# Performance work log

Hardware: AMD Instinct MI355X
Metric: run time of the kernel (lower is better)

The kernel has to match this reference:

```python
import jax, jax.numpy as jnp
import numpy as np

N = 100000
MUL_IN0, MUL_IN1 = 256, 128      # in_irreps: 256x0e + 128x1o  (dim 640)
MUL_S, MUL_G = 512, 256          # hidden: 512x0e scalars, 256x1o gated (+256x0e gates)
MUL_H0 = MUL_S + MUL_G           # 768 l=0 channels produced by lin1/lin2
MUL_OUT0, MUL_OUT1 = 256, 128    # out_irreps: 256x0e + 128x1o (dim 640)
EPS = 1e-5


def _p(key, shape):
    return jax.random.normal(key, shape, dtype=jnp.float32)


def setup_inputs() -> dict:
    key = jax.random.key(0)
    ks = jax.random.split(key, 11)
    return {
        "features": _p(ks[0], (N, MUL_IN0 + 3 * MUL_IN1)),
        "lin1_W0": _p(ks[1], (MUL_IN0, MUL_H0)),
        "lin1_W1": _p(ks[2], (MUL_IN1, MUL_G)),
        "lin2_W0": _p(ks[3], (MUL_S, MUL_H0)),
        "lin2_W1": _p(ks[4], (MUL_G, MUL_G)),
        "lin3_W0": _p(ks[5], (MUL_S, MUL_OUT0)),
        "lin3_W1": _p(ks[6], (MUL_G, MUL_OUT1)),
        "byp_W0": _p(ks[7], (MUL_IN0, MUL_OUT0)),
        "byp_W1": _p(ks[8], (MUL_IN1, MUL_OUT1)),
        "bn_weight": jnp.ones((MUL_OUT0 + MUL_OUT1,), jnp.float32),
        "bn_bias": jnp.zeros((MUL_OUT0,), jnp.float32),
    }


def _irlin(x, mul0_in, mul1_in, W0, W1):
    # e3nn o3.Linear on simplified irreps: independent (block-diagonal) matmul
    # per angular momentum l, with 1/sqrt(fan_in) path normalization.
    n = x.shape[0]
    x0 = x[:, :mul0_in]                              # [n, mul0_in]      l=0
    x1 = x[:, mul0_in:].reshape(n, mul1_in, 3)       # [n, mul1_in, 3]   l=1
    y0 = (x0 @ W0) * np.float32(1.0 / np.sqrt(mul0_in))
    y1 = jnp.einsum('nid,io->nod', x1, W1) * np.float32(1.0 / np.sqrt(mul1_in))
    return jnp.concatenate([y0, y1.reshape(n, -1)], axis=-1)


def _gate(h):
    # e3nn Gate: SiLU on scalars, sigmoid(gates) multiplies each gated l=1 irrep
    n = h.shape[0]
    s = jax.nn.silu(h[:, :MUL_S])
    g = jax.nn.sigmoid(h[:, MUL_S:MUL_S + MUL_G])
    v = h[:, MUL_S + MUL_G:].reshape(n, MUL_G, 3)
    return jnp.concatenate([s, (v * g[:, :, None]).reshape(n, -1)], axis=-1)


def _batchnorm(x, w, b):
    # e3nn BatchNorm (training mode, normalization='component', reduce='mean'):
    # scalars get mean-subtraction + bias; l>0 only per-mul norm scaling.
    n = x.shape[0]
    s = x[:, :MUL_OUT0]
    v = x[:, MUL_OUT0:].reshape(n, MUL_OUT1, 3)
    s = s - s.mean(0)
    s_inv = jax.lax.rsqrt((s * s).mean(0) + EPS)               # [MUL_OUT0]
    s = s * (s_inv * w[:MUL_OUT0]) + b
    v_inv = jax.lax.rsqrt((v * v).mean(-1).mean(0) + EPS)      # [MUL_OUT1]
    v = v * (v_inv * w[MUL_OUT0:])[None, :, None]
    return jnp.concatenate([s, v.reshape(n, -1)], axis=-1)


def reference(features, lin1_W0, lin1_W1, lin2_W0, lin2_W1, lin3_W0, lin3_W1,
              byp_W0, byp_W1, bn_weight, bn_bias):
    h = _irlin(features, MUL_IN0, MUL_IN1, lin1_W0, lin1_W1)   # [N, 1536]
    h = _gate(h)                                               # [N, 1280]
    h = _irlin(h, MUL_S, MUL_G, lin2_W0, lin2_W1)              # [N, 1536]
    h = _gate(h)                                               # [N, 1280]
    out = _irlin(h, MUL_S, MUL_G, lin3_W0, lin3_W1)            # [N, 640]
    out = out + _irlin(features, MUL_IN0, MUL_IN1, byp_W0, byp_W1)
    return _batchnorm(out, bn_weight, bn_bias)
```

## Files before the change

kernel.cpp:

```cpp
#include <hip/hip_runtime.h>

using f32x4 = __attribute__((ext_vector_type(4))) float;
using s16x8 = __attribute__((ext_vector_type(8))) short;

#define NROWS 100000

__device__ __forceinline__ unsigned short f2bf(float f) {
    unsigned int u = __float_as_uint(f);
    u = (u + 0x7fffu + ((u >> 16) & 1u)) >> 16;
    return (unsigned short)u;
}

__device__ __forceinline__ float sigm(float x) { return 1.0f / (1.0f + __expf(-x)); }


__global__ void pack_w(const float* __restrict__ W, unsigned short* __restrict__ Wt,
                       int K, int Nn, float scale) {
    int idx = blockIdx.x * blockDim.x + threadIdx.x;
    if (idx >= K * Nn) return;
    int n = idx / K, k = idx - n * K;
    Wt[idx] = f2bf(W[(size_t)k * Nn + n] * scale);
}

__global__ void pack_x(const float* __restrict__ F, unsigned short* __restrict__ Xs) {
    size_t total = (size_t)NROWS * 640;
    size_t stride = (size_t)gridDim.x * blockDim.x;
    for (size_t idx = (size_t)blockIdx.x * blockDim.x + threadIdx.x; idx < total; idx += stride) {
        size_t n = idx / 640;
        int co = (int)(idx - n * 640);
        int ci = (co < 256) ? co : (256 + 3 * ((co - 256) & 127) + ((co - 256) >> 7));
        Xs[idx] = f2bf(F[n * 640 + ci]);
    }
}

template<int TPW, int CNT, int ABASE>
__device__ __forceinline__ void gemm_seg(f32x4 (&acc)[TPW][2],
        const unsigned short* X, int cin, int row0, int lane,
        const unsigned short* W, int K, int kb, int wrow0) {
    const unsigned short* xp = X + (size_t)(row0 + (lane & 15)) * cin + kb + ((lane >> 4) << 3);
    const unsigned short* wp = W + (size_t)(wrow0 + (lane & 15)) * K + ((lane >> 4) << 3);
    const size_t xstep = (size_t)cin << 4;
    for (int k = 0; k < K; k += 32) {
        s16x8 a0 = *(const s16x8*)(xp + k);
        s16x8 a1 = *(const s16x8*)(xp + xstep + k);
        #pragma unroll
        for (int i = 0; i < CNT; ++i) {
            s16x8 b = *(const s16x8*)(wp + (size_t)(i * 16) * K + k);
            acc[ABASE + i][0] = __builtin_amdgcn_mfma_f32_16x16x32_bf16(a0, b, acc[ABASE + i][0], 0, 0, 0);
            acc[ABASE + i][1] = __builtin_amdgcn_mfma_f32_16x16x32_bf16(a1, b, acc[ABASE + i][1], 0, 0, 0);
        }
    }
}

template<int K0, int K1>
__global__ __launch_bounds__(512, 2) void layer12_kernel(
        const unsigned short* Xin, const unsigned short* __restrict__ W0t,
        const unsigned short* __restrict__ W1t, unsigned short* Out) {
    constexpr int CIN = K0 + 3 * K1;
    __shared__ float gbuf[32][256];
    const int tid = threadIdx.x, wid = tid >> 6, lane = tid & 63;
    const int row0 = blockIdx.x * 32;

    f32x4 acc[12][2];
    const f32x4 vz = {0.f, 0.f, 0.f, 0.f};
    #pragma unroll
    for (int i = 0; i < 12; ++i) { acc[i][0] = vz; acc[i][1] = vz; }

    switch (wid) {
    case 0: gemm_seg<12,12,0>(acc, Xin, CIN, row0, lane, W0t, K0, 0, 0); break;
    case 1: gemm_seg<12,12,0>(acc, Xin, CIN, row0, lane, W0t, K0, 0, 192); break;
    case 2: gemm_seg<12,12,0>(acc, Xin, CIN, row0, lane, W0t, K0, 0, 384); break;
    case 3: gemm_seg<12,12,0>(acc, Xin, CIN, row0, lane, W0t, K0, 0, 576); break;
    case 4: gemm_seg<12,12,0>(acc, Xin, CIN, row0, lane, W1t, K1, K0, 0); break;
    case 5: gemm_seg<12,4,0>(acc, Xin, CIN, row0, lane, W1t, K1, K0, 192);
            gemm_seg<12,8,4>(acc, Xin, CIN, row0, lane, W1t, K1, K0 + K1, 0); break;
    case 6: gemm_seg<12,8,0>(acc, Xin, CIN, row0, lane, W1t, K1, K0 + K1, 128);
            gemm_seg<12,4,8>(acc, Xin, CIN, row0, lane, W1t, K1, K0 + 2 * K1, 0); break;
    case 7: gemm_seg<12,12,0>(acc, Xin, CIN, row0, lane, W1t, K1, K0 + 2 * K1, 64); break;
    }
    __syncthreads();

    const int colg = lane & 15, rbase = (lane >> 4) * 4;
    #pragma unroll
    for (int i = 0; i < 12; ++i) {
        int t = wid * 12 + i;
        if (t < 32) {
            #pragma unroll
            for (int mm = 0; mm < 2; ++mm)
            #pragma unroll
            for (int r = 0; r < 4; ++r) {
                float v = acc[i][mm][r];
                int row = mm * 16 + rbase + r;
                Out[(size_t)(row0 + row) * 1280 + t * 16 + colg] = f2bf(v * sigm(v));
            }
        } else if (t < 48) {
            #pragma unroll
            for (int mm = 0; mm < 2; ++mm)
            #pragma unroll
            for (int r = 0; r < 4; ++r) {
                float v = acc[i][mm][r];
                gbuf[mm * 16 + rbase + r][(t - 32) * 16 + colg] = sigm(v);
            }
        }
    }
    __syncthreads();
    #pragma unroll
    for (int i = 0; i < 12; ++i) {
        int t = wid * 12 + i;
        if (t >= 48) {
            int u = t - 48, d = u >> 4, jj = ((u & 15) << 4) + colg;
            #pragma unroll
            for (int mm = 0; mm < 2; ++mm)
            #pragma unroll
            for (int r = 0; r < 4; ++r) {
                int row = mm * 16 + rbase + r;
                float v = acc[i][mm][r] * gbuf[row][jj];
                Out[(size_t)(row0 + row) * 1280 + 512 + d * 256 + jj] = f2bf(v);
            }
        }
    }
}

__global__ __launch_bounds__(512, 2) void layer3_kernel(
        const unsigned short* G2, const unsigned short* __restrict__ W0t,
        const unsigned short* __restrict__ W1t,
        const unsigned short* __restrict__ Xs,
        const unsigned short* __restrict__ Wb0, const unsigned short* __restrict__ Wb1,
        float* OutF, float* __restrict__ stats) {
    const int tid = threadIdx.x, wid = tid >> 6, lane = tid & 63;
    const int row0 = blockIdx.x * 32;

    f32x4 acc[5][2];
    const f32x4 vz = {0.f, 0.f, 0.f, 0.f};
    #pragma unroll
    for (int i = 0; i < 5; ++i) { acc[i][0] = vz; acc[i][1] = vz; }

    switch (wid) {
    case 0: gemm_seg<5,5,0>(acc, G2, 1280, row0, lane, W0t, 512, 0, 0);
            gemm_seg<5,5,0>(acc, Xs, 640, row0, lane, Wb0, 256, 0, 0); break;
    case 1: gemm_seg<5,5,0>(acc, G2, 1280, row0, lane, W0t, 512, 0, 80);
            gemm_seg<5,5,0>(acc, Xs, 640, row0, lane, Wb0, 256, 0, 80); break;
    case 2: gemm_seg<5,5,0>(acc, G2, 1280, row0, lane, W0t, 512, 0, 160);
            gemm_seg<5,5,0>(acc, Xs, 640, row0, lane, Wb0, 256, 0, 160); break;
    case 3: gemm_seg<5,1,0>(acc, G2, 1280, row0, lane, W0t, 512, 0, 240);
            gemm_seg<5,4,1>(acc, G2, 1280, row0, lane, W1t, 256, 512, 0);
            gemm_seg<5,1,0>(acc, Xs, 640, row0, lane, Wb0, 256, 0, 240);
            gemm_seg<5,4,1>(acc, Xs, 640, row0, lane, Wb1, 128, 256, 0); break;
    case 4: gemm_seg<5,4,0>(acc, G2, 1280, row0, lane, W1t, 256, 512, 64);
            gemm_seg<5,1,4>(acc, G2, 1280, row0, lane, W1t, 256, 768, 0);
            gemm_seg<5,4,0>(acc, Xs, 640, row0, lane, Wb1, 128, 256, 64);
            gemm_seg<5,1,4>(acc, Xs, 640, row0, lane, Wb1, 128, 384, 0); break;
    case 5: gemm_seg<5,5,0>(acc, G2, 1280, row0, lane, W1t, 256, 768, 16);
            gemm_seg<5,5,0>(acc, Xs, 640, row0, lane, Wb1, 128, 384, 16); break;
    case 6: gemm_seg<5,2,0>(acc, G2, 1280, row0, lane, W1t, 256, 768, 96);
            gemm_seg<5,3,2>(acc, G2, 1280, row0, lane, W1t, 256, 1024, 0);
            gemm_seg<5,2,0>(acc, Xs, 640, row0, lane, Wb1, 128, 384, 96);
            gemm_seg<5,3,2>(acc, Xs, 640, row0, lane, Wb1, 128, 512, 0); break;
    case 7: gemm_seg<5,5,0>(acc, G2, 1280, row0, lane, W1t, 256, 1024, 48);
            gemm_seg<5,5,0>(acc, Xs, 640, row0, lane, Wb1, 128, 512, 48); break;
    }
    __syncthreads();

    const int colg = lane & 15, rbase = (lane >> 4) * 4;
    #pragma unroll
    for (int i = 0; i < 5; ++i) {
        int t = wid * 5 + i;
        bool isScalar = t < 16;
        int col;
        if (isScalar) col = t * 16 + colg;
        else { int u = t - 16; col = 256 + (u >> 3) * 128 + ((u & 7) << 4) + colg; }
        float s0 = 0.f, s1 = 0.f;
        #pragma unroll
        for (int mm = 0; mm < 2; ++mm)
        #pragma unroll
        for (int r = 0; r < 4; ++r) {
            float v = acc[i][mm][r];
            OutF[(size_t)(row0 + mm * 16 + rbase + r) * 640 + col] = v;
            s0 += v; s1 += v * v;
        }
        s0 += __shfl_xor(s0, 16); s0 += __shfl_xor(s0, 32);
        s1 += __shfl_xor(s1, 16); s1 += __shfl_xor(s1, 32);
        if (lane < 16) {
            if (isScalar) atomicAdd(&stats[col], s0);
            atomicAdd(&stats[256 + col], s1);
        }
    }
}

__global__ void bn_finalize(const float* __restrict__ stats, const float* __restrict__ bnw,
                            const float* __restrict__ bnb, float* __restrict__ params) {
    int c = threadIdx.x;
    const float invN = 1.0f / (float)NROWS;
    if (c < 256) {
        float mean = stats[c] * invN;
        float var = stats[256 + c] * invN - mean * mean;
        float sc = rsqrtf(var + 1e-5f) * bnw[c];
        params[c] = sc;
        params[256 + c] = bnb[c] - mean * sc;
    } else if (c < 384) {
        int j = c - 256;
        float sv = stats[512 + j] + stats[640 + j] + stats[768 + j];
        float vinv = rsqrtf(sv * (invN * (1.0f / 3.0f)) + 1e-5f) * bnw[256 + j];
        params[512 + j] = vinv;
    }
}

__global__ void bn_apply(const float* __restrict__ OutF, const float* __restrict__ params,
                         float* __restrict__ out) {
    size_t total = (size_t)NROWS * 640;
    size_t stride = (size_t)gridDim.x * blockDim.x * 4;
    for (size_t base = ((size_t)blockIdx.x * blockDim.x + threadIdx.x) * 4; base < total; base += stride) {
        size_t n = base / 640;
        int c0 = (int)(base - n * 640);
        const float* rowp = OutF + n * 640;
        f32x4 o;
        #pragma unroll
        for (int q = 0; q < 4; ++q) {
            int c = c0 + q;
            if (c < 256) {
                o[q] = rowp[c] * params[c] + params[256 + c];
            } else {
                int u = c - 256; int j = u / 3; int d = u - 3 * j;
                o[q] = rowp[256 + d * 128 + j] * params[512 + j];
            }
        }
        *(f32x4*)(out + base) = o;
    }
}

extern "C" void kernel_launch(void* const* d_in, const int* in_sizes, int n_in,
                              void* d_out, int out_size, void* d_ws, size_t ws_size,
                              hipStream_t stream) {
    const float* features = (const float*)d_in[0];
    const float* l1w0 = (const float*)d_in[1];
    const float* l1w1 = (const float*)d_in[2];
    const float* l2w0 = (const float*)d_in[3];
    const float* l2w1 = (const float*)d_in[4];
    const float* l3w0 = (const float*)d_in[5];
    const float* l3w1 = (const float*)d_in[6];
    const float* bw0  = (const float*)d_in[7];
    const float* bw1  = (const float*)d_in[8];
    const float* bnw  = (const float*)d_in[9];
    const float* bnb  = (const float*)d_in[10];
    float* out = (float*)d_out;
    char* ws = (char*)d_ws;

    unsigned short* W10 = (unsigned short*)(ws + 0);
    unsigned short* W11 = (unsigned short*)(ws + 393216);
    unsigned short* W20 = (unsigned short*)(ws + 458752);
    unsigned short* W21 = (unsigned short*)(ws + 1245184);
    unsigned short* W30 = (unsigned short*)(ws + 1376256);
    unsigned short* W31 = (unsigned short*)(ws + 1638400);
    unsigned short* WB0 = (unsigned short*)(ws + 1703936);
    unsigned short* WB1 = (unsigned short*)(ws + 1835008);
    float* stats  = (float*)(ws + 1867776);
    float* params = (float*)(ws + 1871360);
    unsigned short* Xs = (unsigned short*)(ws + 2097152);
    unsigned short* G  = (unsigned short*)(ws + 130097152);
    float* Gf = (float*)G;

    hipMemsetAsync(stats, 0, 896 * sizeof(float), stream);

    const float s_inv16   = 0.0625f;
    const float s_inv128  = 0.08838834764831845f;
    const float s_inv512  = 0.04419417382415922f;

    pack_w<<<768, 256, 0, stream>>>(l1w0, W10, 256, 768, s_inv16);
    pack_w<<<128, 256, 0, stream>>>(l1w1, W11, 128, 256, s_inv128);
    pack_w<<<1536, 256, 0, stream>>>(l2w0, W20, 512, 768, s_inv512);
    pack_w<<<256, 256, 0, stream>>>(l2w1, W21, 256, 256, s_inv16);
    pack_w<<<512, 256, 0, stream>>>(l3w0, W30, 512, 256, s_inv512);
    pack_w<<<128, 256, 0, stream>>>(l3w1, W31, 256, 128, s_inv16);
    pack_w<<<256, 256, 0, stream>>>(bw0, WB0, 256, 256, s_inv16);
    pack_w<<<64, 256, 0, stream>>>(bw1, WB1, 128, 128, s_inv128);
    pack_x<<<8192, 256, 0, stream>>>(features, Xs);

    layer12_kernel<256, 128><<<3125, 512, 0, stream>>>(Xs, W10, W11, G);
    layer12_kernel<512, 256><<<3125, 512, 0, stream>>>(G, W20, W21, G);
    layer3_kernel<<<3125, 512, 0, stream>>>(G, W30, W31, Xs, WB0, WB1, Gf, stats);
    bn_finalize<<<1, 512, 0, stream>>>(stats, bnw, bnb, params);
    bn_apply<<<4096, 256, 0, stream>>>(Gf, params, out);
}
```

Measured before the change: 2.235 ms.

## Restructure GEMM layers to 16-row tiles with per-wave gate/vector ownership

The layer kernels drop from 32-row to 16-row blocks, and the work is split so each wave owns matching scalar, gate and vector output columns. The gate multiply can then happen in registers, with no shared-memory gbuf or second barrier. The eight weight-packing launches are merged into one kernel, and pack_x now writes four values at a time. Smaller per-wave accumulator sets allow a higher occupancy target (launch bounds 4), but each loaded weight tile is now reused over 16 rows instead of 32, which doubles weight traffic per row.

```diff
diff --git a/kernel.cpp b/kernel.cpp
--- a/kernel.cpp
+++ b/kernel.cpp
@@ -2,6 +2,7 @@
 
 using f32x4 = __attribute__((ext_vector_type(4))) float;
 using s16x8 = __attribute__((ext_vector_type(8))) short;
+using u32x2 = __attribute__((ext_vector_type(2))) unsigned int;
 
 #define NROWS 100000
 
@@ -13,177 +14,242 @@
 
 __device__ __forceinline__ float sigm(float x) { return 1.0f / (1.0f + __expf(-x)); }
 
-
-__global__ void pack_w(const float* __restrict__ W, unsigned short* __restrict__ Wt,
-                       int K, int Nn, float scale) {
+#define MFMA(a, b, c) __builtin_amdgcn_mfma_f32_16x16x32_bf16((a), (b), (c), 0, 0, 0)
+
+__device__ __forceinline__ void packseg(const float* __restrict__ W, unsigned short* __restrict__ dst,
+                                        int i, int logK, int Nn, float scale) {
+    int n = i >> logK, k = i & ((1 << logK) - 1);
+    dst[i] = f2bf(W[(size_t)k * Nn + n] * scale);
+}
+
+__global__ void pack_w_all(const float* __restrict__ w10, const float* __restrict__ w11,
+                           const float* __restrict__ w20, const float* __restrict__ w21,
+                           const float* __restrict__ w30, const float* __restrict__ w31,
+                           const float* __restrict__ wb0, const float* __restrict__ wb1,
+                           unsigned short* __restrict__ out) {
+    const float S16  = 0.0625f;
+    const float S128 = 0.08838834764831845f;
+    const float S512 = 0.04419417382415922f;
     int idx = blockIdx.x * blockDim.x + threadIdx.x;
-    if (idx >= K * Nn) return;
-    int n = idx / K, k = idx - n * K;
-    Wt[idx] = f2bf(W[(size_t)k * Nn + n] * scale);
+    if (idx < 196608)        packseg(w10, out,          idx,          8, 768, S16);
+    else if (idx < 229376)   packseg(w11, out + 196608, idx - 196608, 7, 256, S128);
+    else if (idx < 622592)   packseg(w20, out + 229376, idx - 229376, 9, 768, S512);
+    else if (idx < 688128)   packseg(w21, out + 622592, idx - 622592, 8, 256, S16);
+    else if (idx < 819200)   packseg(w30, out + 688128, idx - 688128, 9, 256, S512);
+    else if (idx < 851968)   packseg(w31, out + 819200, idx - 819200, 8, 128, S16);
+    else if (idx < 917504)   packseg(wb0, out + 851968, idx - 851968, 8, 256, S16);
+    else if (idx < 933888)   packseg(wb1, out + 917504, idx - 917504, 7, 128, S128);
 }
 
 __global__ void pack_x(const float* __restrict__ F, unsigned short* __restrict__ Xs) {
-    size_t total = (size_t)NROWS * 640;
+    size_t total = (size_t)NROWS * 160;
     size_t stride = (size_t)gridDim.x * blockDim.x;
-    for (size_t idx = (size_t)blockIdx.x * blockDim.x + threadIdx.x; idx < total; idx += stride) {
-        size_t n = idx / 640;
-        int co = (int)(idx - n * 640);
-        int ci = (co < 256) ? co : (256 + 3 * ((co - 256) & 127) + ((co - 256) >> 7));
-        Xs[idx] = f2bf(F[n * 640 + ci]);
-    }
-}
-
-template<int TPW, int CNT, int ABASE>
-__device__ __forceinline__ void gemm_seg(f32x4 (&acc)[TPW][2],
-        const unsigned short* X, int cin, int row0, int lane,
-        const unsigned short* W, int K, int kb, int wrow0) {
-    const unsigned short* xp = X + (size_t)(row0 + (lane & 15)) * cin + kb + ((lane >> 4) << 3);
-    const unsigned short* wp = W + (size_t)(wrow0 + (lane & 15)) * K + ((lane >> 4) << 3);
-    const size_t xstep = (size_t)cin << 4;
-    for (int k = 0; k < K; k += 32) {
-        s16x8 a0 = *(const s16x8*)(xp + k);
-        s16x8 a1 = *(const s16x8*)(xp + xstep + k);
-        #pragma unroll
-        for (int i = 0; i < CNT; ++i) {
-            s16x8 b = *(const s16x8*)(wp + (size_t)(i * 16) * K + k);
-            acc[ABASE + i][0] = __builtin_amdgcn_mfma_f32_16x16x32_bf16(a0, b, acc[ABASE + i][0], 0, 0, 0);
-            acc[ABASE + i][1] = __builtin_amdgcn_mfma_f32_16x16x32_bf16(a1, b, acc[ABASE + i][1], 0, 0, 0);
-        }
+    for (size_t g = (size_t)blockIdx.x * blockDim.x + threadIdx.x; g < total; g += stride) {
+        size_t n = g / 160;
+        int c0 = (int)(g - n * 160) * 4;
+        const float* row = F + n * 640;
+        unsigned short o[4];
+        if (c0 < 256) {
+            f32x4 v = *(const f32x4*)(row + c0);
+            #pragma unroll
+            for (int q = 0; q < 4; ++q) o[q] = f2bf(v[q]);
+        } else {
+            int u = c0 - 256;
+            int d = u >> 7, j = u & 127;
+            int base = 256 + 3 * j + d;
+            #pragma unroll
+            for (int q = 0; q < 4; ++q) o[q] = f2bf(row[base + 3 * q]);
+        }
+        u32x2 pk;
+        pk[0] = (unsigned int)o[0] | ((unsigned int)o[1] << 16);
+        pk[1] = (unsigned int)o[2] | ((unsigned int)o[3] << 16);
+        *(u32x2*)(Xs + n * 640 + c0) = pk;
     }
 }
 
 template<int K0, int K1>
-__global__ __launch_bounds__(512, 2) void layer12_kernel(
-        const unsigned short* Xin, const unsigned short* __restrict__ W0t,
-        const unsigned short* __restrict__ W1t, unsigned short* Out) {
+__global__ __launch_bounds__(512, 4) void layer12_v2(
+        const unsigned short* Xin,
+        const unsigned short* __restrict__ W0t,
+        const unsigned short* __restrict__ W1t,
+        unsigned short* Out) {
     constexpr int CIN = K0 + 3 * K1;
-    __shared__ float gbuf[32][256];
     const int tid = threadIdx.x, wid = tid >> 6, lane = tid & 63;
-    const int row0 = blockIdx.x * 32;
-
-    f32x4 acc[12][2];
+    const int row0 = blockIdx.x * 16;
+    const int lrow = lane & 15;
+    const int lk = (lane >> 4) << 3;
+
+    f32x4 accS[4], accG[2], accV[2][3];
     const f32x4 vz = {0.f, 0.f, 0.f, 0.f};
     #pragma unroll
-    for (int i = 0; i < 12; ++i) { acc[i][0] = vz; acc[i][1] = vz; }
-
-    switch (wid) {
-    case 0: gemm_seg<12,12,0>(acc, Xin, CIN, row0, lane, W0t, K0, 0, 0); break;
-    case 1: gemm_seg<12,12,0>(acc, Xin, CIN, row0, lane, W0t, K0, 0, 192); break;
-    case 2: gemm_seg<12,12,0>(acc, Xin, CIN, row0, lane, W0t, K0, 0, 384); break;
-    case 3: gemm_seg<12,12,0>(acc, Xin, CIN, row0, lane, W0t, K0, 0, 576); break;
-    case 4: gemm_seg<12,12,0>(acc, Xin, CIN, row0, lane, W1t, K1, K0, 0); break;
-    case 5: gemm_seg<12,4,0>(acc, Xin, CIN, row0, lane, W1t, K1, K0, 192);
-            gemm_seg<12,8,4>(acc, Xin, CIN, row0, lane, W1t, K1, K0 + K1, 0); break;
-    case 6: gemm_seg<12,8,0>(acc, Xin, CIN, row0, lane, W1t, K1, K0 + K1, 128);
-            gemm_seg<12,4,8>(acc, Xin, CIN, row0, lane, W1t, K1, K0 + 2 * K1, 0); break;
-    case 7: gemm_seg<12,12,0>(acc, Xin, CIN, row0, lane, W1t, K1, K0 + 2 * K1, 64); break;
-    }
+    for (int i = 0; i < 4; ++i) accS[i] = vz;
+    #pragma unroll
+    for (int i = 0; i < 2; ++i) {
+        accG[i] = vz;
+        #pragma unroll
+        for (int d = 0; d < 3; ++d) accV[i][d] = vz;
+    }
+
+    const unsigned short* xp = Xin + (size_t)(row0 + lrow) * CIN + lk;
+    const unsigned short* bs = W0t + (size_t)(64 * wid + lrow) * K0 + lk;
+    const unsigned short* bg = W0t + (size_t)(512 + 32 * wid + lrow) * K0 + lk;
+
+    #pragma unroll
+    for (int ks = 0; ks < K0 / 32; ++ks) {
+        const int k = ks * 32;
+        s16x8 a = *(const s16x8*)(xp + k);
+        #pragma unroll
+        for (int i = 0; i < 4; ++i) {
+            s16x8 b = *(const s16x8*)(bs + (size_t)(16 * i) * K0 + k);
+            accS[i] = MFMA(a, b, accS[i]);
+        }
+        #pragma unroll
+        for (int i = 0; i < 2; ++i) {
+            s16x8 b = *(const s16x8*)(bg + (size_t)(16 * i) * K0 + k);
+            accG[i] = MFMA(a, b, accG[i]);
+        }
+    }
+
+    const unsigned short* bv = W1t + (size_t)(32 * wid + lrow) * K1 + lk;
+    #pragma unroll
+    for (int ks = 0; ks < K1 / 32; ++ks) {
+        const int k = ks * 32;
+        s16x8 a0 = *(const s16x8*)(xp + K0 + k);
+        s16x8 a1 = *(const s16x8*)(xp + K0 + K1 + k);
+        s16x8 a2 = *(const s16x8*)(xp + K0 + 2 * K1 + k);
+        #pragma unroll
+        for (int i = 0; i < 2; ++i) {
+            s16x8 b = *(const s16x8*)(bv + (size_t)(16 * i) * K1 + k);
+            accV[i][0] = MFMA(a0, b, accV[i][0]);
+            accV[i][1] = MFMA(a1, b, accV[i][1]);
+            accV[i][2] = MFMA(a2, b, accV[i][2]);
+        }
+    }
+
     __syncthreads();
 
-    const int colg = lane & 15, rbase = (lane >> 4) * 4;
-    #pragma unroll
-    for (int i = 0; i < 12; ++i) {
-        int t = wid * 12 + i;
-        if (t < 32) {
-            #pragma unroll
-            for (int mm = 0; mm < 2; ++mm)
-            #pragma unroll
-            for (int r = 0; r < 4; ++r) {
-                float v = acc[i][mm][r];
-                int row = mm * 16 + rbase + r;
-                Out[(size_t)(row0 + row) * 1280 + t * 16 + colg] = f2bf(v * sigm(v));
-            }
-        } else if (t < 48) {
-            #pragma unroll
-            for (int mm = 0; mm < 2; ++mm)
-            #pragma unroll
-            for (int r = 0; r < 4; ++r) {
-                float v = acc[i][mm][r];
-                gbuf[mm * 16 + rbase + r][(t - 32) * 16 + colg] = sigm(v);
-            }
-        }
-    }
-    __syncthreads();
-    #pragma unroll
-    for (int i = 0; i < 12; ++i) {
-        int t = wid * 12 + i;
-        if (t >= 48) {
-            int u = t - 48, d = u >> 4, jj = ((u & 15) << 4) + colg;
-            #pragma unroll
-            for (int mm = 0; mm < 2; ++mm)
-            #pragma unroll
-            for (int r = 0; r < 4; ++r) {
-                int row = mm * 16 + rbase + r;
-                float v = acc[i][mm][r] * gbuf[row][jj];
-                Out[(size_t)(row0 + row) * 1280 + 512 + d * 256 + jj] = f2bf(v);
-            }
-        }
-    }
-}
-
-__global__ __launch_bounds__(512, 2) void layer3_kernel(
-        const unsigned short* G2, const unsigned short* __restrict__ W0t,
+    const int colg = lane & 15;
+    const int rbase = (lane >> 4) * 4;
+    #pragma unroll
+    for (int r = 0; r < 4; ++r) {
+        const size_t ro = (size_t)(row0 + rbase + r) * 1280;
+        #pragma unroll
+        for (int i = 0; i < 4; ++i) {
+            float v = accS[i][r];
+            Out[ro + 64 * wid + 16 * i + colg] = f2bf(v * sigm(v));
+        }
+        #pragma unroll
+        for (int i = 0; i < 2; ++i) {
+            float g = sigm(accG[i][r]);
+            #pragma unroll
+            for (int d = 0; d < 3; ++d) {
+                Out[ro + 512 + 256 * d + 32 * wid + 16 * i + colg] = f2bf(accV[i][d][r] * g);
+            }
+        }
+    }
+}
+
+__global__ __launch_bounds__(512, 4) void layer3_v2(
+        const unsigned short* G2,
+        const unsigned short* __restrict__ W0t,
         const unsigned short* __restrict__ W1t,
         const unsigned short* __restrict__ Xs,
-        const unsigned short* __restrict__ Wb0, const unsigned short* __restrict__ Wb1,
+        const unsigned short* __restrict__ Wb0,
+        const unsigned short* __restrict__ Wb1,
         float* OutF, float* __restrict__ stats) {
     const int tid = threadIdx.x, wid = tid >> 6, lane = tid & 63;
-    const int row0 = blockIdx.x * 32;
-
-    f32x4 acc[5][2];
+    const int row0 = blockIdx.x * 16;
+    const int lrow = lane & 15, lk = (lane >> 4) << 3;
+
+    f32x4 accS[2], accV[3];
     const f32x4 vz = {0.f, 0.f, 0.f, 0.f};
-    #pragma unroll
-    for (int i = 0; i < 5; ++i) { acc[i][0] = vz; acc[i][1] = vz; }
-
-    switch (wid) {
-    case 0: gemm_seg<5,5,0>(acc, G2, 1280, row0, lane, W0t, 512, 0, 0);
-            gemm_seg<5,5,0>(acc, Xs, 640, row0, lane, Wb0, 256, 0, 0); break;
-    case 1: gemm_seg<5,5,0>(acc, G2, 1280, row0, lane, W0t, 512, 0, 80);
-            gemm_seg<5,5,0>(acc, Xs, 640, row0, lane, Wb0, 256, 0, 80); break;
-    case 2: gemm_seg<5,5,0>(acc, G2, 1280, row0, lane, W0t, 512, 0, 160);
-            gemm_seg<5,5,0>(acc, Xs, 640, row0, lane, Wb0, 256, 0, 160); break;
-    case 3: gemm_seg<5,1,0>(acc, G2, 1280, row0, lane, W0t, 512, 0, 240);
-            gemm_seg<5,4,1>(acc, G2, 1280, row0, lane, W1t, 256, 512, 0);
-            gemm_seg<5,1,0>(acc, Xs, 640, row0, lane, Wb0, 256, 0, 240);
-            gemm_seg<5,4,1>(acc, Xs, 640, row0, lane, Wb1, 128, 256, 0); break;
-    case 4: gemm_seg<5,4,0>(acc, G2, 1280, row0, lane, W1t, 256, 512, 64);
-            gemm_seg<5,1,4>(acc, G2, 1280, row0, lane, W1t, 256, 768, 0);
-            gemm_seg<5,4,0>(acc, Xs, 640, row0, lane, Wb1, 128, 256, 64);
-            gemm_seg<5,1,4>(acc, Xs, 640, row0, lane, Wb1, 128, 384, 0); break;
-    case 5: gemm_seg<5,5,0>(acc, G2, 1280, row0, lane, W1t, 256, 768, 16);
-            gemm_seg<5,5,0>(acc, Xs, 640, row0, lane, Wb1, 128, 384, 16); break;
-    case 6: gemm_seg<5,2,0>(acc, G2, 1280, row0, lane, W1t, 256, 768, 96);
-            gemm_seg<5,3,2>(acc, G2, 1280, row0, lane, W1t, 256, 1024, 0);
-            gemm_seg<5,2,0>(acc, Xs, 640, row0, lane, Wb1, 128, 384, 96);
-            gemm_seg<5,3,2>(acc, Xs, 640, row0, lane, Wb1, 128, 512, 0); break;
-    case 7: gemm_seg<5,5,0>(acc, G2, 1280, row0, lane, W1t, 256, 1024, 48);
-            gemm_seg<5,5,0>(acc, Xs, 640, row0, lane, Wb1, 128, 512, 48); break;
-    }
+    accS[0] = vz; accS[1] = vz; accV[0] = vz; accV[1] = vz; accV[2] = vz;
+
+    const unsigned short* gp = G2 + (size_t)(row0 + lrow) * 1280 + lk;
+    const unsigned short* xp = Xs + (size_t)(row0 + lrow) * 640 + lk;
+
+    {
+        const unsigned short* b0 = W0t + (size_t)(32 * wid + lrow) * 512 + lk;
+        #pragma unroll
+        for (int ks = 0; ks < 16; ++ks) {
+            const int k = ks * 32;
+            s16x8 a = *(const s16x8*)(gp + k);
+            #pragma unroll
+            for (int i = 0; i < 2; ++i) {
+                s16x8 b = *(const s16x8*)(b0 + (size_t)(16 * i) * 512 + k);
+                accS[i] = MFMA(a, b, accS[i]);
+            }
+        }
+    }
+    {
+        const unsigned short* c0 = Wb0 + (size_t)(32 * wid + lrow) * 256 + lk;
+        #pragma unroll
+        for (int ks = 0; ks < 8; ++ks) {
+            const int k = ks * 32;
+            s16x8 a = *(const s16x8*)(xp + k);
+            #pragma unroll
+            for (int i = 0; i < 2; ++i) {
+                s16x8 b = *(const s16x8*)(c0 + (size_t)(16 * i) * 256 + k);
+                accS[i] = MFMA(a, b, accS[i]);
+            }
+        }
+    }
+    {
+        const unsigned short* b1 = W1t + (size_t)(16 * wid + lrow) * 256 + lk;
+        #pragma unroll
+        for (int ks = 0; ks < 8; ++ks) {
+            const int k = ks * 32;
+            s16x8 b = *(const s16x8*)(b1 + k);
+            #pragma unroll
+            for (int d = 0; d < 3; ++d) {
+                s16x8 a = *(const s16x8*)(gp + 512 + 256 * d + k);
+                accV[d] = MFMA(a, b, accV[d]);
+            }
+        }
+    }
+    {
+        const unsigned short* c1 = Wb1 + (size_t)(16 * wid + lrow) * 128 + lk;
+        #pragma unroll
+        for (int ks = 0; ks < 4; ++ks) {
+            const int k = ks * 32;
+            s16x8 b = *(const s16x8*)(c1 + k);
+            #pragma unroll
+            for (int d = 0; d < 3; ++d) {
+                s16x8 a = *(const s16x8*)(xp + 256 + 128 * d + k);
+                accV[d] = MFMA(a, b, accV[d]);
+            }
+        }
+    }
+
     __syncthreads();
 
     const int colg = lane & 15, rbase = (lane >> 4) * 4;
     #pragma unroll
-    for (int i = 0; i < 5; ++i) {
-        int t = wid * 5 + i;
-        bool isScalar = t < 16;
-        int col;
-        if (isScalar) col = t * 16 + colg;
-        else { int u = t - 16; col = 256 + (u >> 3) * 128 + ((u & 7) << 4) + colg; }
+    for (int i = 0; i < 2; ++i) {
+        const int col = 32 * wid + 16 * i + colg;
         float s0 = 0.f, s1 = 0.f;
         #pragma unroll
-        for (int mm = 0; mm < 2; ++mm)
-        #pragma unroll
         for (int r = 0; r < 4; ++r) {
-            float v = acc[i][mm][r];
-            OutF[(size_t)(row0 + mm * 16 + rbase + r) * 640 + col] = v;
+            float v = accS[i][r];
+            OutF[(size_t)(row0 + rbase + r) * 640 + col] = v;
             s0 += v; s1 += v * v;
         }
         s0 += __shfl_xor(s0, 16); s0 += __shfl_xor(s0, 32);
         s1 += __shfl_xor(s1, 16); s1 += __shfl_xor(s1, 32);
-        if (lane < 16) {
-            if (isScalar) atomicAdd(&stats[col], s0);
-            atomicAdd(&stats[256 + col], s1);
-        }
+        if (lane < 16) { atomicAdd(&stats[col], s0); atomicAdd(&stats[256 + col], s1); }
+    }
+    #pragma unroll
+    for (int d = 0; d < 3; ++d) {
+        const int j = 16 * wid + colg;
+        float s1 = 0.f;
+        #pragma unroll
+        for (int r = 0; r < 4; ++r) {
+            float v = accV[d][r];
+            OutF[(size_t)(row0 + rbase + r) * 640 + 256 + 128 * d + j] = v;
+            s1 += v * v;
+        }
+        s1 += __shfl_xor(s1, 16); s1 += __shfl_xor(s1, 32);
+        if (lane < 16) atomicAdd(&stats[512 + 128 * d + j], s1);
     }
 }
 
@@ -245,39 +311,29 @@
     float* out = (float*)d_out;
     char* ws = (char*)d_ws;
 
-    unsigned short* W10 = (unsigned short*)(ws + 0);
-    unsigned short* W11 = (unsigned short*)(ws + 393216);
-    unsigned short* W20 = (unsigned short*)(ws + 458752);
-    unsigned short* W21 = (unsigned short*)(ws + 1245184);
-    unsigned short* W30 = (unsigned short*)(ws + 1376256);
-    unsigned short* W31 = (unsigned short*)(ws + 1638400);
-    unsigned short* WB0 = (unsigned short*)(ws + 1703936);
-    unsigned short* WB1 = (unsigned short*)(ws + 1835008);
-    float* stats  = (float*)(ws + 1867776);
-    float* params = (float*)(ws + 1871360);
+    unsigned short* Wt = (unsigned short*)(ws + 0);
+    unsigned short* W10 = Wt + 0;
+    unsigned short* W11 = Wt + 196608;
+    unsigned short* W20 = Wt + 229376;
+    unsigned short* W21 = Wt + 622592;
+    unsigned short* W30 = Wt + 688128;
+    unsigned short* W31 = Wt + 819200;
+    unsigned short* WB0 = Wt + 851968;
+    unsigned short* WB1 = Wt + 917504;
+    float* stats  = (float*)(ws + 1900544);
+    float* params = (float*)(ws + 1904128);
     unsigned short* Xs = (unsigned short*)(ws + 2097152);
     unsigned short* G  = (unsigned short*)(ws + 130097152);
     float* Gf = (float*)G;
 
     hipMemsetAsync(stats, 0, 896 * sizeof(float), stream);
 
-    const float s_inv16   = 0.0625f;
-    const float s_inv128  = 0.08838834764831845f;
-    const float s_inv512  = 0.04419417382415922f;
-
-    pack_w<<<768, 256, 0, stream>>>(l1w0, W10, 256, 768, s_inv16);
-    pack_w<<<128, 256, 0, stream>>>(l1w1, W11, 128, 256, s_inv128);
-    pack_w<<<1536, 256, 0, stream>>>(l2w0, W20, 512, 768, s_inv512);
-    pack_w<<<256, 256, 0, stream>>>(l2w1, W21, 256, 256, s_inv16);
-    pack_w<<<512, 256, 0, stream>>>(l3w0, W30, 512, 256, s_inv512);
-    pack_w<<<128, 256, 0, stream>>>(l3w1, W31, 256, 128, s_inv16);
-    pack_w<<<256, 256, 0, stream>>>(bw0, WB0, 256, 256, s_inv16);
-    pack_w<<<64, 256, 0, stream>>>(bw1, WB1, 128, 128, s_inv128);
-    pack_x<<<8192, 256, 0, stream>>>(features, Xs);
-
-    layer12_kernel<256, 128><<<3125, 512, 0, stream>>>(Xs, W10, W11, G);
-    layer12_kernel<512, 256><<<3125, 512, 0, stream>>>(G, W20, W21, G);
-    layer3_kernel<<<3125, 512, 0, stream>>>(G, W30, W31, Xs, WB0, WB1, Gf, stats);
+    pack_w_all<<<3648, 256, 0, stream>>>(l1w0, l1w1, l2w0, l2w1, l3w0, l3w1, bw0, bw1, Wt);
+    pack_x<<<4096, 256, 0, stream>>>(features, Xs);
+
+    layer12_v2<256, 128><<<6250, 512, 0, stream>>>(Xs, W10, W11, G);
+    layer12_v2<512, 256><<<6250, 512, 0, stream>>>(G, W20, W21, G);
+    layer3_v2<<<6250, 512, 0, stream>>>(G, W30, W31, Xs, WB0, WB1, Gf, stats);
     bn_finalize<<<1, 512, 0, stream>>>(stats, bnw, bnb, params);
     bn_apply<<<4096, 256, 0, stream>>>(Gf, params, out);
 }
```

Result: slower. 2.594 ms (+16.1%).
